# Kernel tuning notes

Measured on AMD Instinct MI355X. Metric: run time of the kernel, lower is better.

The kernel has to match this reference:

```python
import jax, jax.numpy as jnp
import numpy as np

N_NODES = 50000
N_EDGES = 800000
IN_DIM = 13
HID = 64
LAYER_DIMS = [(IN_DIM, HID), (HID, HID), (HID, HID), (HID, HID), (HID, 1)]


def setup_inputs() -> dict:
    key = jax.random.key(0)
    ks = jax.random.split(key, 20)
    x = jax.random.normal(ks[0], (N_NODES, IN_DIM), dtype=jnp.float32)
    edge_index = jax.random.randint(ks[1], (2, N_EDGES), 0, N_NODES)
    edge_weight = jax.random.uniform(ks[2], (N_EDGES,), dtype=jnp.float32)
    inp = {"x": x, "edge_index": edge_index, "edge_weight": edge_weight}
    for i, (di, do) in enumerate(LAYER_DIMS):
        s = 1.0 / np.sqrt(di)
        inp[f"Wrel{i}"] = (jax.random.normal(ks[3 + 3 * i], (di, do)) * s).astype(jnp.float32)
        inp[f"brel{i}"] = jnp.zeros((do,), dtype=jnp.float32)
        inp[f"Wroot{i}"] = (jax.random.normal(ks[4 + 3 * i], (di, do)) * s).astype(jnp.float32)
    return inp


def _graph_conv(x, src, dst, ew, Wrel, brel, Wroot):
    # PyG GraphConv: out = lin_rel(sum_{j in N(i)} w_e * x_j) + lin_root(x_i)
    msgs = ew[:, None] * x[src]                      # [E, d_in] gather
    aggr = jax.ops.segment_sum(msgs, dst, num_segments=N_NODES)  # [N, d_in]
    return aggr @ Wrel + brel + x @ Wroot


def reference(x, edge_index, edge_weight,
              Wrel0, brel0, Wroot0,
              Wrel1, brel1, Wroot1,
              Wrel2, brel2, Wroot2,
              Wrel3, brel3, Wroot3,
              Wrel4, brel4, Wroot4):
    src, dst = edge_index[0], edge_index[1]  # source_to_target flow
    params = [
        (Wrel0, brel0, Wroot0),
        (Wrel1, brel1, Wroot1),
        (Wrel2, brel2, Wroot2),
        (Wrel3, brel3, Wroot3),
        (Wrel4, brel4, Wroot4),
    ]
    h = x
    for Wr, br, Ws in params[:-1]:
        h = jax.nn.relu(_graph_conv(h, src, dst, edge_weight, Wr, br, Ws))
    Wr, br, Ws = params[-1]
    h = _graph_conv(h, src, dst, edge_weight, Wr, br, Ws)
    return jax.nn.sigmoid(h)  # [N, 1]
```

## Files before the change

kernel.cpp:

```cpp
#include <hip/hip_runtime.h>
#include <math.h>

#define N_NODES 50000
#define N_EDGES 800000
#define NBUCKET 196
#define CHUNK 4096
#define NCHUNK 196
#define SCAN_N (NBUCKET * NCHUNK)
#define SB_A 151
#define SB_B 196
#define EPT 16
#define CAP_FINE 8192
#define MAXEPAD (N_EDGES + N_NODES * 8)

typedef __attribute__((ext_vector_type(8))) _Float16 f16x8;
typedef __attribute__((ext_vector_type(4))) _Float16 f16x4;
typedef __attribute__((ext_vector_type(4))) float f32x4;

__device__ __forceinline__ int roundup8(int v) { return (v + 7) & ~7; }


__device__ __forceinline__ int block_excl_scan(int v, int* wsum) {
    int t = threadIdx.x, lane = t & 63, w = t >> 6;
    int sc = v;
    #pragma unroll
    for (int o = 1; o < 64; o <<= 1) {
        int u = __shfl_up(sc, o, 64);
        if (lane >= o) sc += u;
    }
    if (lane == 63) wsum[w] = sc;
    __syncthreads();
    int add = 0;
    #pragma unroll
    for (int j = 0; j < 4; ++j) if (j < w) add += wsum[j];
    return add + sc - v;
}


__global__ void hist_kernel(const int* __restrict__ dst, int* __restrict__ h,
                            int* __restrict__ counts) {
    __shared__ int hist[NBUCKET];
    for (int i = threadIdx.x; i < NBUCKET; i += 256) hist[i] = 0;
    __syncthreads();
    int base = blockIdx.x * CHUNK;
    int n = min(CHUNK, N_EDGES - base);
    for (int k = threadIdx.x; k < n; k += 256) {
        int d = dst[base + k];
        atomicAdd(&hist[d >> 8], 1);
        atomicAdd(&counts[d], 1);
    }
    __syncthreads();
    for (int i = threadIdx.x; i < NBUCKET; i += 256)
        h[i * NCHUNK + blockIdx.x] = hist[i];
}


__global__ void scan_blocks_dual(int* __restrict__ h, const int* __restrict__ counts,
                                 int* __restrict__ offs, int* __restrict__ blocksums) {
    __shared__ int wsum[4];
    int bid = blockIdx.x, t = threadIdx.x;
    if (bid < SB_A) {
        int i = bid * 256 + t;
        int v = (i < SCAN_N) ? h[i] : 0;
        int e = block_excl_scan(v, wsum);
        if (i < SCAN_N) h[i] = e;
        if (t == 255) blocksums[bid] = e + v;
    } else {
        int j = (bid - SB_A) * 256 + t;
        int v = (j < N_NODES) ? roundup8(counts[j]) : 0;
        int e = block_excl_scan(v, wsum);
        if (j < N_NODES) offs[j] = e;
        if (t == 255) blocksums[bid] = e + v;
    }
}

__global__ void scan_mid(const int* __restrict__ blocksums, int* __restrict__ blockoffs) {
    __shared__ int wsum[4];
    int base = (blockIdx.x == 0) ? 0 : SB_A;
    int n = (blockIdx.x == 0) ? SB_A : SB_B;
    int t = threadIdx.x;
    int v = (t < n) ? blocksums[base + t] : 0;
    int e = block_excl_scan(v, wsum);
    if (t < n) blockoffs[base + t] = e;
}

__global__ void scan_add_dual(int* __restrict__ h, int* __restrict__ offs,
                              const int* __restrict__ counts,
                              const int* __restrict__ blockoffs) {
    int bid = blockIdx.x, t = threadIdx.x;
    if (bid < SB_A) {
        int i = bid * 256 + t;
        if (i < SCAN_N) h[i] += blockoffs[bid];
    } else {
        int j = (bid - SB_A) * 256 + t;
        if (j < N_NODES) {
            int v = offs[j] + blockoffs[bid];
            offs[j] = v;
            if (j == N_NODES - 1) offs[N_NODES] = v + roundup8(counts[j]);
        }
    }
}


__launch_bounds__(256, 4)
__global__ void scatter_coarse(const int* __restrict__ src, const int* __restrict__ dst,
                               const float* __restrict__ ew, const int* __restrict__ hs,
                               int2* __restrict__ ecoarse) {
    __shared__ int cnt[NBUCKET];
    __shared__ int excl[NBUCKET];
    __shared__ int cur[NBUCKET];
    __shared__ int gbase[NBUCKET];
    __shared__ int wsum[4];
    __shared__ int2 stage[CHUNK];

    int t = threadIdx.x;
    int base = blockIdx.x * CHUNK;
    int n = min(CHUNK, N_EDGES - base);

    for (int i = t; i < NBUCKET; i += 256) {
        cnt[i] = 0;
        gbase[i] = hs[i * NCHUNK + blockIdx.x];
    }
    __syncthreads();

    int rx[EPT];
    float rw[EPT];
    #pragma unroll
    for (int j = 0; j < EPT; ++j) {
        int k = t + j * 256;
        if (k < n) {
            int e = base + k;
            int d = dst[e];
            rx[j] = (d << 16) | src[e];
            rw[j] = ew[e];
            atomicAdd(&cnt[d >> 8], 1);
        }
    }
    __syncthreads();

    {
        int v = (t < NBUCKET) ? cnt[t] : 0;
        int e = block_excl_scan(v, wsum);
        if (t < NBUCKET) { excl[t] = e; cur[t] = e; }
    }
    __syncthreads();

    #pragma unroll
    for (int j = 0; j < EPT; ++j) {
        int k = t + j * 256;
        if (k < n) {
            int b = ((unsigned)rx[j]) >> 24;
            int p = atomicAdd(&cur[b], 1);
            stage[p] = make_int2(rx[j], __float_as_int(rw[j]));
        }
    }
    __syncthreads();

    for (int k = t; k < n; k += 256) {
        int2 r = stage[k];
        int b = ((unsigned)r.x) >> 24;
        ecoarse[gbase[b] + (k - excl[b])] = r;
    }
}


__launch_bounds__(256)
__global__ void fine_sort(const int* __restrict__ h, const int* __restrict__ offs,
                          const int2* __restrict__ ecoarse, int2* __restrict__ esrt) {
    int b = blockIdx.x, t = threadIdx.x;
    __shared__ int cur[256];
    __shared__ int2 stage[CAP_FINE];
    int bstartU = h[b * NCHUNK];
    int bendU = (b == NBUCKET - 1) ? N_EDGES : h[(b + 1) * NCHUNK];
    int nbU = bendU - bstartU;
    int P = offs[b << 8];
    int nodeEnd = min((b + 1) << 8, N_NODES);
    int plen = offs[nodeEnd] - P;
    int dstv = (b << 8) + t;
    cur[t] = (dstv < N_NODES) ? offs[dstv] - P : 0;
    __syncthreads();
    if (plen <= CAP_FINE) {
        for (int k = t; k < plen; k += 256) stage[k] = make_int2(0, 0);
        __syncthreads();
        for (int k = t; k < nbU; k += 256) {
            int2 r = ecoarse[bstartU + k];
            int d = (((unsigned)r.x) >> 16) & 255;
            int p = atomicAdd(&cur[d], 1);
            stage[p] = make_int2(r.x & 0xFFFF, r.y);
        }
        __syncthreads();
        for (int k = t; k < plen; k += 256) esrt[P + k] = stage[k];
    } else {
        for (int k = t; k < plen; k += 256) esrt[P + k] = make_int2(0, 0);
        __syncthreads();
        for (int k = t; k < nbU; k += 256) {
            int2 r = ecoarse[bstartU + k];
            int d = (((unsigned)r.x) >> 16) & 255;
            int p = atomicAdd(&cur[d], 1);
            esrt[P + p] = make_int2(r.x & 0xFFFF, r.y);
        }
    }
}


__global__ void wconv(const float* __restrict__ W1r, const float* __restrict__ W1o,
                      const float* __restrict__ W2r, const float* __restrict__ W2o,
                      const float* __restrict__ W3r, const float* __restrict__ W3o,
                      _Float16* __restrict__ wfrag) {
    int b = blockIdx.x, t = threadIdx.x;
    const float* Wr = (b == 0) ? W1r : (b == 1) ? W2r : W3r;
    const float* Wo = (b == 0) ? W1o : (b == 1) ? W2o : W3o;
    _Float16* out = wfrag + (size_t)b * 8192;
    for (int i = t; i < 1024; i += 256) {
        int frag = i >> 6, lane = i & 63;
        int m = frag >> 3, ct = (frag >> 1) & 3, ks = frag & 1;
        int col = ct * 16 + (lane & 15);
        int kb = ks * 32 + (lane >> 4) * 8;
        const float* W = m ? Wo : Wr;
        f16x8 v;
        #pragma unroll
        for (int j = 0; j < 8; ++j) v[j] = (_Float16)W[(kb + j) * 64 + col];
        *(f16x8*)&out[(size_t)i * 8] = v;
    }
}


__device__ __forceinline__ float bcast(float v, int k) {
    return __int_as_float(__builtin_amdgcn_readlane(__float_as_int(v), k));
}


__launch_bounds__(256)
__global__ void layer0_fused(const int* __restrict__ offs, const int2* __restrict__ esrt,
                             const float* __restrict__ x, const float* __restrict__ Wrel,
                             const float* __restrict__ bias, const float* __restrict__ Wroot,
                             _Float16* __restrict__ h0) {
    int wid = (blockIdx.x * blockDim.x + threadIdx.x) >> 6;
    int lane = threadIdx.x & 63;
    float wr[13], wo[13];
    #pragma unroll
    for (int k = 0; k < 13; ++k) {
        wr[k] = Wrel[k * 64 + lane];
        wo[k] = Wroot[k * 64 + lane];
    }
    float bc = bias[lane];
    int q = lane >> 4, f = lane & 15;
    int beg = offs[wid], end = offs[wid + 1];
    float acc = 0.f;
    bool fv = (f < 13);
    for (int i = beg + q; i < end; i += 8) {
        int2 e0 = esrt[i], e1 = esrt[i + 4];
        float v0 = fv ? x[(size_t)e0.x * 13 + f] : 0.f;
        float v1 = fv ? x[(size_t)e1.x * 13 + f] : 0.f;
        acc = fmaf(__int_as_float(e0.y), v0, acc);
        acc = fmaf(__int_as_float(e1.y), v1, acc);
    }
    acc += __shfl_xor(acc, 16, 64);
    acc += __shfl_xor(acc, 32, 64);
    float hv = (lane < 13) ? x[(size_t)wid * 13 + lane] : 0.f;
    float a0 = bc, a1 = 0.f, a2 = 0.f, a3 = 0.f;
    #pragma unroll
    for (int k = 0; k + 2 <= 13; k += 2) {
        a0 = fmaf(bcast(acc, k), wr[k], a0);
        a1 = fmaf(bcast(hv, k), wo[k], a1);
        a2 = fmaf(bcast(acc, k + 1), wr[k + 1], a2);
        a3 = fmaf(bcast(hv, k + 1), wo[k + 1], a3);
    }
    a0 = fmaf(bcast(acc, 12), wr[12], a0);
    a1 = fmaf(bcast(hv, 12), wo[12], a1);
    float o = fmaxf((a0 + a2) + (a1 + a3), 0.f);
    h0[(size_t)wid * 64 + lane] = (_Float16)o;
}


template <bool FINAL>
__launch_bounds__(256)
__global__ void layer_fused(const int* __restrict__ offs, const int2* __restrict__ esrt,
                            const _Float16* __restrict__ hin, const _Float16* __restrict__ wfrag_l,
                            const float* __restrict__ bias, _Float16* __restrict__ hout,
                            const float* __restrict__ Wrel4, const float* __restrict__ Wroot4,
                            float* __restrict__ z, float* __restrict__ root) {
    __shared__ __align__(16) _Float16 bfrag[16][64][8];
    __shared__ __align__(16) float aggrT[32][68];
    __shared__ __align__(16) _Float16 hrootT[32][72];
    __shared__ float zpart[4][32], rpart[4][32];
    int t = threadIdx.x;
    int rowbase = blockIdx.x * 32;

    {
        const int4* s = (const int4*)wfrag_l;
        int4* d = (int4*)&bfrag[0][0][0];
        #pragma unroll
        for (int i = 0; i < 4; ++i) d[t + 256 * i] = s[t + 256 * i];
    }
    {
        int row = t >> 3, c8 = (t & 7) * 8;
        int gr = min(rowbase + row, N_NODES - 1);
        *(int4*)&hrootT[row][c8] = *(const int4*)&hin[(size_t)gr * 64 + c8];
    }

    int qw = t >> 4, f4 = t & 15;
    #pragma unroll
    for (int rr = 0; rr < 2; ++rr) {
        int node = rowbase + qw + rr * 16;
        float4 acc = make_float4(0.f, 0.f, 0.f, 0.f);
        if (node < N_NODES) {
            int beg = offs[node], end = offs[node + 1];
            for (int i = beg; i < end; i += 4) {
                int2 e0 = esrt[i], e1 = esrt[i + 1], e2 = esrt[i + 2], e3 = esrt[i + 3];
                f16x4 v0 = *((const f16x4*)(hin + (size_t)e0.x * 64) + f4);
                f16x4 v1 = *((const f16x4*)(hin + (size_t)e1.x * 64) + f4);
                f16x4 v2 = *((const f16x4*)(hin + (size_t)e2.x * 64) + f4);
                f16x4 v3 = *((const f16x4*)(hin + (size_t)e3.x * 64) + f4);
                float w0 = __int_as_float(e0.y), w1 = __int_as_float(e1.y);
                float w2 = __int_as_float(e2.y), w3 = __int_as_float(e3.y);
                acc.x = fmaf(w0, (float)v0[0], acc.x); acc.y = fmaf(w0, (float)v0[1], acc.y);
                acc.z = fmaf(w0, (float)v0[2], acc.z); acc.w = fmaf(w0, (float)v0[3], acc.w);
                acc.x = fmaf(w1, (float)v1[0], acc.x); acc.y = fmaf(w1, (float)v1[1], acc.y);
                acc.z = fmaf(w1, (float)v1[2], acc.z); acc.w = fmaf(w1, (float)v1[3], acc.w);
                acc.x = fmaf(w2, (float)v2[0], acc.x); acc.y = fmaf(w2, (float)v2[1], acc.y);
                acc.z = fmaf(w2, (float)v2[2], acc.z); acc.w = fmaf(w2, (float)v2[3], acc.w);
                acc.x = fmaf(w3, (float)v3[0], acc.x); acc.y = fmaf(w3, (float)v3[1], acc.y);
                acc.z = fmaf(w3, (float)v3[2], acc.z); acc.w = fmaf(w3, (float)v3[3], acc.w);
            }
        }
        *(float4*)&aggrT[qw + rr * 16][f4 * 4] = acc;
    }
    __syncthreads();

    int w = t >> 6, lane = t & 63;
    int r = lane & 15, koff = (lane >> 4) * 8;
    float bc = bias[w * 16 + r];
    float w4rv = 0.f, w4ov = 0.f;
    if (FINAL) { w4rv = Wrel4[w * 16 + r]; w4ov = Wroot4[w * 16 + r]; }

    #pragma unroll
    for (int g = 0; g < 2; ++g) {
        int lr = g * 16 + r;
        f16x8 Ah[2], Al[2], Ar[2];
        #pragma unroll
        for (int ks = 0; ks < 2; ++ks) {
            float4 a0 = *(const float4*)&aggrT[lr][ks * 32 + koff];
            float4 a1 = *(const float4*)&aggrT[lr][ks * 32 + koff + 4];
            float vv[8] = {a0.x, a0.y, a0.z, a0.w, a1.x, a1.y, a1.z, a1.w};
            f16x8 hi, lo;
            #pragma unroll
            for (int j = 0; j < 8; ++j) {
                _Float16 hh = (_Float16)vv[j];
                hi[j] = hh;
                lo[j] = (_Float16)(vv[j] - (float)hh);
            }
            Ah[ks] = hi;
            Al[ks] = lo;
            Ar[ks] = *(const f16x8*)&hrootT[lr][ks * 32 + koff];
        }
        f32x4 acc = {bc, bc, bc, bc};
        #pragma unroll
        for (int ks = 0; ks < 2; ++ks) {
            f16x8 br = *(const f16x8*)&bfrag[(0 * 4 + w) * 2 + ks][lane][0];
            f16x8 bo = *(const f16x8*)&bfrag[(1 * 4 + w) * 2 + ks][lane][0];
            acc = __builtin_amdgcn_mfma_f32_16x16x32_f16(Ah[ks], br, acc, 0, 0, 0);
            acc = __builtin_amdgcn_mfma_f32_16x16x32_f16(Al[ks], br, acc, 0, 0, 0);
            acc = __builtin_amdgcn_mfma_f32_16x16x32_f16(Ar[ks], bo, acc, 0, 0, 0);
        }
        if (FINAL) {
            #pragma unroll
            for (int j = 0; j < 4; ++j) {
                float o = fmaxf(acc[j], 0.f);
                float zz = o * w4rv, rv = o * w4ov;
                #pragma unroll
                for (int m = 1; m < 16; m <<= 1) {
                    zz += __shfl_xor(zz, m, 64);
                    rv += __shfl_xor(rv, m, 64);
                }
                if (r == 0) {
                    int lrow = g * 16 + (lane >> 4) * 4 + j;
                    zpart[w][lrow] = zz;
                    rpart[w][lrow] = rv;
                }
            }
        } else {
            #pragma unroll
            for (int j = 0; j < 4; ++j) {
                int row = rowbase + g * 16 + (lane >> 4) * 4 + j;
                if (row < N_NODES)
                    hout[(size_t)row * 64 + w * 16 + r] = (_Float16)fmaxf(acc[j], 0.f);
            }
        }
    }
    if (FINAL) {
        __syncthreads();
        if (t < 32) {
            int row = rowbase + t;
            if (row < N_NODES) {
                z[row] = zpart[0][t] + zpart[1][t] + zpart[2][t] + zpart[3][t];
                root[row] = rpart[0][t] + rpart[1][t] + rpart[2][t] + rpart[3][t];
            }
        }
    }
}


__launch_bounds__(256)
__global__ void final_aggr(const int* __restrict__ offs, const int2* __restrict__ esrt,
                           const float* __restrict__ z, const float* __restrict__ root,
                           const float* __restrict__ b4, float* __restrict__ out) {
    int tid = blockIdx.x * blockDim.x + threadIdx.x;
    int node = tid >> 2, g = tid & 3;
    if (node >= N_NODES) return;
    int beg = offs[node], end = offs[node + 1];
    float a = 0.f;
    for (int i = beg + g; i < end; i += 8) {
        int2 e0 = esrt[i], e1 = esrt[i + 4];
        a = fmaf(__int_as_float(e0.y), z[e0.x], a);
        a = fmaf(__int_as_float(e1.y), z[e1.x], a);
    }
    a += __shfl_xor(a, 1, 64);
    a += __shfl_xor(a, 2, 64);
    if (g == 0) {
        float v = a + b4[0] + root[node];
        out[node] = 1.f / (1.f + expf(-v));
    }
}


extern "C" void kernel_launch(void* const* d_in, const int* in_sizes, int n_in,
                              void* d_out, int out_size, void* d_ws, size_t ws_size,
                              hipStream_t stream) {
    const float* x = (const float*)d_in[0];
    const int* eidx = (const int*)d_in[1];
    const float* ew = (const float*)d_in[2];
    const float* Wrel[5];
    const float* brel[5];
    const float* Wroot[5];
    for (int i = 0; i < 5; ++i) {
        Wrel[i] = (const float*)d_in[3 + 3 * i];
        brel[i] = (const float*)d_in[4 + 3 * i];
        Wroot[i] = (const float*)d_in[5 + 3 * i];
    }
    const int* src = eidx;
    const int* dst = eidx + N_EDGES;
    float* out = (float*)d_out;

    char* ws = (char*)d_ws;
    size_t off = 0;
    auto alloc = [&](size_t bytes) -> void* {
        void* p = ws + off;
        off = (off + bytes + 255) & ~(size_t)255;
        return p;
    };
    int* h = (int*)alloc((size_t)(SCAN_N + 256) * 4);
    int* blocksums = (int*)alloc(512 * 4);
    int* blockoffs = (int*)alloc(512 * 4);
    int* counts = (int*)alloc((size_t)N_NODES * 4);
    int* offs = (int*)alloc((size_t)(N_NODES + 1) * 4);
    int2* esrt = (int2*)alloc((size_t)MAXEPAD * 8);
    _Float16* h0 = (_Float16*)alloc((size_t)N_NODES * 64 * 2);
    _Float16* h1 = (_Float16*)alloc((size_t)N_NODES * 64 * 2);
    _Float16* wfrag = (_Float16*)alloc((size_t)3 * 8192 * 2);
    float* z = (float*)alloc((size_t)N_NODES * 4);
    float* root = (float*)alloc((size_t)N_NODES * 4);
    int2* ecoarse = (int2*)h0;
    (void)ws_size; (void)in_sizes; (void)n_in; (void)out_size;

    hipMemsetAsync(counts, 0, (size_t)N_NODES * 4, stream);
    hist_kernel<<<NCHUNK, 256, 0, stream>>>(dst, h, counts);
    scan_blocks_dual<<<SB_A + SB_B, 256, 0, stream>>>(h, counts, offs, blocksums);
    scan_mid<<<2, 256, 0, stream>>>(blocksums, blockoffs);
    scan_add_dual<<<SB_A + SB_B, 256, 0, stream>>>(h, offs, counts, blockoffs);
    scatter_coarse<<<NCHUNK, 256, 0, stream>>>(src, dst, ew, h, ecoarse);
    fine_sort<<<NBUCKET, 256, 0, stream>>>(h, offs, ecoarse, esrt);

    wconv<<<3, 256, 0, stream>>>(Wrel[1], Wroot[1], Wrel[2], Wroot[2], Wrel[3], Wroot[3], wfrag);

    const int NODE_BLOCKS = N_NODES * 64 / 256;
    const int FB = (N_NODES + 31) / 32;

    layer0_fused<<<NODE_BLOCKS, 256, 0, stream>>>(offs, esrt, x, Wrel[0], brel[0], Wroot[0], h0);

    layer_fused<false><<<FB, 256, 0, stream>>>(offs, esrt, h0, wfrag, brel[1], h1,
                                               nullptr, nullptr, nullptr, nullptr);
    layer_fused<false><<<FB, 256, 0, stream>>>(offs, esrt, h1, wfrag + 8192, brel[2], h0,
                                               nullptr, nullptr, nullptr, nullptr);
    layer_fused<true><<<FB, 256, 0, stream>>>(offs, esrt, h0, wfrag + 16384, brel[3], nullptr,
                                              Wrel[4], Wroot[4], z, root);

    final_aggr<<<(N_NODES * 4 + 255) / 256, 256, 0, stream>>>(offs, esrt, z, root, brel[4], out);
}
```

Before: 199.5 us.

## Pad edge segments to 4 and gather 16-byte fp16 rows in hidden-layer aggregation

```diff
diff --git a/kernel.cpp b/kernel.cpp
--- a/kernel.cpp
+++ b/kernel.cpp
@@ -11,13 +11,12 @@
 #define SB_B 196
 #define EPT 16
 #define CAP_FINE 8192
-#define MAXEPAD (N_EDGES + N_NODES * 8)
+#define MAXEPAD (N_EDGES + N_NODES * 4)
 
 typedef __attribute__((ext_vector_type(8))) _Float16 f16x8;
-typedef __attribute__((ext_vector_type(4))) _Float16 f16x4;
 typedef __attribute__((ext_vector_type(4))) float f32x4;
 
-__device__ __forceinline__ int roundup8(int v) { return (v + 7) & ~7; }
+__device__ __forceinline__ int roundup4(int v) { return (v + 3) & ~3; }
 
 
 __device__ __forceinline__ int block_excl_scan(int v, int* wsum) {
@@ -67,7 +66,7 @@
         if (t == 255) blocksums[bid] = e + v;
     } else {
         int j = (bid - SB_A) * 256 + t;
-        int v = (j < N_NODES) ? roundup8(counts[j]) : 0;
+        int v = (j < N_NODES) ? roundup4(counts[j]) : 0;
         int e = block_excl_scan(v, wsum);
         if (j < N_NODES) offs[j] = e;
         if (t == 255) blocksums[bid] = e + v;
@@ -96,7 +95,7 @@
         if (j < N_NODES) {
             int v = offs[j] + blockoffs[bid];
             offs[j] = v;
-            if (j == N_NODES - 1) offs[N_NODES] = v + roundup8(counts[j]);
+            if (j == N_NODES - 1) offs[N_NODES] = v + roundup4(counts[j]);
         }
     }
 }
@@ -248,12 +247,18 @@
     int beg = offs[wid], end = offs[wid + 1];
     float acc = 0.f;
     bool fv = (f < 13);
-    for (int i = beg + q; i < end; i += 8) {
+    int i = beg + q;
+    for (; i + 4 < end; i += 8) {
         int2 e0 = esrt[i], e1 = esrt[i + 4];
         float v0 = fv ? x[(size_t)e0.x * 13 + f] : 0.f;
         float v1 = fv ? x[(size_t)e1.x * 13 + f] : 0.f;
         acc = fmaf(__int_as_float(e0.y), v0, acc);
         acc = fmaf(__int_as_float(e1.y), v1, acc);
+    }
+    if (i < end) {
+        int2 e = esrt[i];
+        float v = fv ? x[(size_t)e.x * 13 + f] : 0.f;
+        acc = fmaf(__int_as_float(e.y), v, acc);
     }
     acc += __shfl_xor(acc, 16, 64);
     acc += __shfl_xor(acc, 32, 64);
@@ -299,32 +304,34 @@
         *(int4*)&hrootT[row][c8] = *(const int4*)&hin[(size_t)gr * 64 + c8];
     }
 
-    int qw = t >> 4, f4 = t & 15;
+    int qw = t >> 4, l = t & 15;
+    int hi8 = l >> 3, f8 = l & 7;
     #pragma unroll
     for (int rr = 0; rr < 2; ++rr) {
         int node = rowbase + qw + rr * 16;
-        float4 acc = make_float4(0.f, 0.f, 0.f, 0.f);
+        float a[8] = {0.f, 0.f, 0.f, 0.f, 0.f, 0.f, 0.f, 0.f};
         if (node < N_NODES) {
             int beg = offs[node], end = offs[node + 1];
             for (int i = beg; i < end; i += 4) {
-                int2 e0 = esrt[i], e1 = esrt[i + 1], e2 = esrt[i + 2], e3 = esrt[i + 3];
-                f16x4 v0 = *((const f16x4*)(hin + (size_t)e0.x * 64) + f4);
-                f16x4 v1 = *((const f16x4*)(hin + (size_t)e1.x * 64) + f4);
-                f16x4 v2 = *((const f16x4*)(hin + (size_t)e2.x * 64) + f4);
-                f16x4 v3 = *((const f16x4*)(hin + (size_t)e3.x * 64) + f4);
-                float w0 = __int_as_float(e0.y), w1 = __int_as_float(e1.y);
-                float w2 = __int_as_float(e2.y), w3 = __int_as_float(e3.y);
-                acc.x = fmaf(w0, (float)v0[0], acc.x); acc.y = fmaf(w0, (float)v0[1], acc.y);
-                acc.z = fmaf(w0, (float)v0[2], acc.z); acc.w = fmaf(w0, (float)v0[3], acc.w);
-                acc.x = fmaf(w1, (float)v1[0], acc.x); acc.y = fmaf(w1, (float)v1[1], acc.y);
-                acc.z = fmaf(w1, (float)v1[2], acc.z); acc.w = fmaf(w1, (float)v1[3], acc.w);
-                acc.x = fmaf(w2, (float)v2[0], acc.x); acc.y = fmaf(w2, (float)v2[1], acc.y);
-                acc.z = fmaf(w2, (float)v2[2], acc.z); acc.w = fmaf(w2, (float)v2[3], acc.w);
-                acc.x = fmaf(w3, (float)v3[0], acc.x); acc.y = fmaf(w3, (float)v3[1], acc.y);
-                acc.z = fmaf(w3, (float)v3[2], acc.z); acc.w = fmaf(w3, (float)v3[3], acc.w);
+                int4 p0 = *(const int4*)(esrt + i);
+                int4 p1 = *(const int4*)(esrt + i + 2);
+                int s0 = hi8 ? p0.z : p0.x;
+                int s1 = hi8 ? p1.z : p1.x;
+                float w0 = __int_as_float(hi8 ? p0.w : p0.y);
+                float w1 = __int_as_float(hi8 ? p1.w : p1.y);
+                f16x8 r0 = *(const f16x8*)(hin + (size_t)s0 * 64 + f8 * 8);
+                f16x8 r1 = *(const f16x8*)(hin + (size_t)s1 * 64 + f8 * 8);
+                #pragma unroll
+                for (int j = 0; j < 8; ++j) {
+                    a[j] = fmaf(w0, (float)r0[j], a[j]);
+                    a[j] = fmaf(w1, (float)r1[j], a[j]);
+                }
             }
         }
-        *(float4*)&aggrT[qw + rr * 16][f4 * 4] = acc;
+        #pragma unroll
+        for (int j = 0; j < 8; ++j) a[j] += __shfl_xor(a[j], 8, 64);
+        float4 wv = make_float4(a[hi8 * 4 + 0], a[hi8 * 4 + 1], a[hi8 * 4 + 2], a[hi8 * 4 + 3]);
+        *(float4*)&aggrT[qw + rr * 16][f8 * 8 + hi8 * 4] = wv;
     }
     __syncthreads();
 
@@ -410,10 +417,15 @@
     if (node >= N_NODES) return;
     int beg = offs[node], end = offs[node + 1];
     float a = 0.f;
-    for (int i = beg + g; i < end; i += 8) {
+    int i = beg + g;
+    for (; i + 4 < end; i += 8) {
         int2 e0 = esrt[i], e1 = esrt[i + 4];
         a = fmaf(__int_as_float(e0.y), z[e0.x], a);
         a = fmaf(__int_as_float(e1.y), z[e1.x], a);
+    }
+    if (i < end) {
+        int2 e = esrt[i];
+        a = fmaf(__int_as_float(e.y), z[e.x], a);
     }
     a += __shfl_xor(a, 1, 64);
     a += __shfl_xor(a, 2, 64);
```

Result: faster. 193.3 us (-3.1%).
